# Kernel tuning notes

Measured on AMD Instinct MI355X. Metric: run time of the kernel, lower is better.

The kernel has to match this reference:

```python
import jax, jax.numpy as jnp
import numpy as np

HIDDEN = 128
SIGMA_A = 15.0
FACTOR_A = 180.0 / (SIGMA_A * np.pi)  # 180/(sigma_a*pi)


def _sinusoidal_embedding(indices, d_model):
    # torch: omegas = idx.view(-1,1,1)*div_term.view(1,-1,1); cat([sin,cos],dim=2)
    # -> interleaved [sin0, cos0, sin1, cos1, ...]
    div_term = jnp.exp(jnp.arange(0, d_model, 2, dtype=jnp.float32) * (-np.log(10000.0) / d_model))
    omegas = indices[..., None] * div_term  # (*, d/2)
    emb = jnp.stack([jnp.sin(omegas), jnp.cos(omegas)], axis=-1)  # (*, d/2, 2)
    return emb.reshape(*indices.shape, d_model)


def setup_inputs() -> dict:
    key = jax.random.key(0)
    k1, k2, k3 = jax.random.split(key, 3)
    B, N = 1, 1024
    points = jax.random.normal(k1, (B, N, 3), dtype=jnp.float32)
    normals = jax.random.normal(k2, (B, N, 3), dtype=jnp.float32)
    W = jax.random.normal(k3, (HIDDEN, HIDDEN), dtype=jnp.float32) / np.sqrt(HIDDEN)
    b = jnp.zeros((HIDDEN,), dtype=jnp.float32)
    return {"points": points, "normals": normals, "W": W, "b": b}


def reference(points, normals, W, b):
    # pairwise angle between normal_i (ref) and normal_j (anc), k=1 so mean over k is a no-op
    ref = normals[:, :, None, :]   # (B,N,1,3) -> n_i
    anc = normals[:, None, :, :]   # (B,1,N,3) -> n_j
    cross = jnp.cross(ref, anc)                    # (B,N,N,3)
    sin_v = jnp.linalg.norm(cross, axis=-1)        # (B,N,N)
    cos_v = jnp.sum(ref * anc, axis=-1)            # (B,N,N)
    angles = jnp.arctan2(sin_v, cos_v)
    a_indices = angles * FACTOR_A
    a_emb = _sinusoidal_embedding(a_indices, HIDDEN)  # (B,N,N,HIDDEN)
    a_emb = jax.lax.stop_gradient(a_emb)  # torch: no_grad + detach
    return a_emb @ W.T + b                # nn.Linear
```

## Files before the change

kernel.cpp:

```cpp
#include <hip/hip_runtime.h>
#include <math.h>


#define N_PTS 1024
#define HID   128
#define K_TAB 127
#define A_MAX 12.0f
#define T_OF_ANGLE 40.1070456591f
#define NEG_LOG1E4_OVER_128 (-0.0719557841f)

__global__ __launch_bounds__(128) void build_table(
        const float* __restrict__ W,
        const float* __restrict__ b,
        float* __restrict__ T) {
    __shared__ float ss[64], sc[64];
    const int t = blockIdx.x;
    const float a = (float)t * (A_MAX / (float)(K_TAB - 1));
    const int k = threadIdx.x;
    if (k < 64) {
        float omega = expf((float)(2 * k) * NEG_LOG1E4_OVER_128);
        ss[k] = sinf(a * omega);
        sc[k] = cosf(a * omega);
    }
    __syncthreads();
    float acc = b[k];
    const float* wrow = W + k * HID;
#pragma unroll 8
    for (int m = 0; m < 64; ++m) {
        acc += ss[m] * wrow[2 * m] + sc[m] * wrow[2 * m + 1];
    }
    T[t * HID + k] = acc;
}

__global__ __launch_bounds__(256) void fused_out(
        const float* __restrict__ normals,
        const float* __restrict__ T,
        float* __restrict__ out) {
    __shared__ float lt[K_TAB * HID];
    for (int idx = threadIdx.x; idx < (K_TAB * HID) / 4; idx += 256)
        ((float4*)lt)[idx] = ((const float4*)T)[idx];
    __syncthreads();

    const int lane = threadIdx.x & 63;
    const int half = lane >> 5;
    const int l32  = lane & 31;
    const int gwave = (blockIdx.x * 256 + threadIdx.x) >> 6;
    const int nwave = (gridDim.x * 256) >> 6;

    for (int base = gwave * 64; base < N_PTS * N_PTS; base += nwave * 64) {
        const int p = base + lane;
        const int i = p >> 10;
        const int j = p & 1023;
        float ax = normals[3 * i],  ay = normals[3 * i + 1], az = normals[3 * i + 2];
        float bx = normals[3 * j],  by = normals[3 * j + 1], bz = normals[3 * j + 2];
        float cx = ay * bz - az * by;
        float cy = az * bx - ax * bz;
        float cz = ax * by - ay * bx;
        float sv = sqrtf(cx * cx + cy * cy + cz * cz);
        float cv = ax * bx + ay * by + az * bz;
        float tval = atan2f(sv, cv) * T_OF_ANGLE;

        float* orow = out + (size_t)(base + half) * HID + l32 * 4;
#pragma unroll 4
        for (int k = 0; k < 32; ++k) {
            float t = __shfl(tval, 2 * k + half, 64);
            int idx = (int)t;
            idx = idx > K_TAB - 2 ? K_TAB - 2 : idx;
            float frac = t - (float)idx;
            const float4 v0 = *(const float4*)(lt + idx * HID + l32 * 4);
            const float4 v1 = *(const float4*)(lt + idx * HID + HID + l32 * 4);
            float4 r;
            r.x = fmaf(frac, v1.x - v0.x, v0.x);
            r.y = fmaf(frac, v1.y - v0.y, v0.y);
            r.z = fmaf(frac, v1.z - v0.z, v0.z);
            r.w = fmaf(frac, v1.w - v0.w, v0.w);
            *(float4*)orow = r;
            orow += 2 * HID;
        }
    }
}

extern "C" void kernel_launch(void* const* d_in, const int* in_sizes, int n_in,
                              void* d_out, int out_size, void* d_ws, size_t ws_size,
                              hipStream_t stream) {
    const float* normals = (const float*)d_in[1];
    const float* W       = (const float*)d_in[2];
    const float* b       = (const float*)d_in[3];
    float* out           = (float*)d_out;

    float* T = (float*)d_ws;

    build_table<<<K_TAB, 128, 0, stream>>>(W, b, T);
    fused_out<<<512, 256, 0, stream>>>(normals, T, out);
}
```

Baseline: 523.3 us.

## Store lookup table in fp16 LDS, interpolate with half2, restructure loop

Converts the shared-memory interpolation table to fp16, which halves LDS footprint and read bandwidth, and does the lerp with packed half2 FMA. The grid grows to 1024 blocks with a fixed 4-iteration outer loop, and launch bounds are set for higher occupancy. Per-point indices and fractions are now precomputed and broadcast with readlane instead of shuffles. This trades accuracy (fp16 table values and fractions) for lower LDS pressure and more blocks resident per CU, while the 4 MB-per-row fp32 output writes remain the main cost.

```diff
diff --git a/kernel.cpp b/kernel.cpp
--- a/kernel.cpp
+++ b/kernel.cpp
@@ -1,4 +1,5 @@
 #include <hip/hip_runtime.h>
+#include <hip/hip_fp16.h>
 #include <math.h>
 
 
@@ -8,6 +9,8 @@
 #define A_MAX 12.0f
 #define T_OF_ANGLE 40.1070456591f
 #define NEG_LOG1E4_OVER_128 (-0.0719557841f)
+#define GRID_B 1024
+#define OUTER  4
 
 __global__ __launch_bounds__(128) void build_table(
         const float* __restrict__ W,
@@ -32,49 +35,74 @@
     T[t * HID + k] = acc;
 }
 
-__global__ __launch_bounds__(256) void fused_out(
+__global__ __launch_bounds__(256, 4) void fused_out(
         const float* __restrict__ normals,
         const float* __restrict__ T,
         float* __restrict__ out) {
-    __shared__ float lt[K_TAB * HID];
-    for (int idx = threadIdx.x; idx < (K_TAB * HID) / 4; idx += 256)
-        ((float4*)lt)[idx] = ((const float4*)T)[idx];
+    __shared__ __half lt[K_TAB * HID];
+    for (int c = threadIdx.x; c < (K_TAB * HID) / 4; c += 256) {
+        float4 v = ((const float4*)T)[c];
+        ((__half2*)lt)[2 * c]     = __floats2half2_rn(v.x, v.y);
+        ((__half2*)lt)[2 * c + 1] = __floats2half2_rn(v.z, v.w);
+    }
     __syncthreads();
 
-    const int lane = threadIdx.x & 63;
-    const int half = lane >> 5;
-    const int l32  = lane & 31;
+    const int lane  = threadIdx.x & 63;
+    const int hsel  = lane >> 5;
+    const int l32   = lane & 31;
     const int gwave = (blockIdx.x * 256 + threadIdx.x) >> 6;
-    const int nwave = (gridDim.x * 256) >> 6;
+    const int STRIDE = GRID_B * 4 * 64;
 
-    for (int base = gwave * 64; base < N_PTS * N_PTS; base += nwave * 64) {
-        const int p = base + lane;
+    int rowb_[OUTER];
+    int frb_[OUTER];
+#pragma unroll
+    for (int o = 0; o < OUTER; ++o) {
+        const int p = gwave * 64 + o * STRIDE + lane;
         const int i = p >> 10;
         const int j = p & 1023;
-        float ax = normals[3 * i],  ay = normals[3 * i + 1], az = normals[3 * i + 2];
-        float bx = normals[3 * j],  by = normals[3 * j + 1], bz = normals[3 * j + 2];
+        float ax = normals[3 * i], ay = normals[3 * i + 1], az = normals[3 * i + 2];
+        float bx = normals[3 * j], by = normals[3 * j + 1], bz = normals[3 * j + 2];
         float cx = ay * bz - az * by;
         float cy = az * bx - ax * bz;
         float cz = ax * by - ay * bx;
         float sv = sqrtf(cx * cx + cy * cy + cz * cz);
         float cv = ax * bx + ay * by + az * bz;
-        float tval = atan2f(sv, cv) * T_OF_ANGLE;
+        float t  = atan2f(sv, cv) * T_OF_ANGLE;
+        int idx = (int)t;
+        idx = idx > K_TAB - 2 ? K_TAB - 2 : idx;
+        float frac = t - (float)idx;
+        rowb_[o] = idx * (HID * 2);
+        __half2 f2 = __float2half2_rn(frac);
+        frb_[o] = __builtin_bit_cast(int, f2);
+    }
 
-        float* orow = out + (size_t)(base + half) * HID + l32 * 4;
-#pragma unroll 4
+    const char* ltb = (const char*)lt;
+    const int laneoff = l32 * 8;
+#pragma unroll
+    for (int o = 0; o < OUTER; ++o) {
+        float* orow = out + (size_t)(gwave * 64 + o * STRIDE + hsel) * HID + l32 * 4;
+#pragma unroll
         for (int k = 0; k < 32; ++k) {
-            float t = __shfl(tval, 2 * k + half, 64);
-            int idx = (int)t;
-            idx = idx > K_TAB - 2 ? K_TAB - 2 : idx;
-            float frac = t - (float)idx;
-            const float4 v0 = *(const float4*)(lt + idx * HID + l32 * 4);
-            const float4 v1 = *(const float4*)(lt + idx * HID + HID + l32 * 4);
-            float4 r;
-            r.x = fmaf(frac, v1.x - v0.x, v0.x);
-            r.y = fmaf(frac, v1.y - v0.y, v0.y);
-            r.z = fmaf(frac, v1.z - v0.z, v0.z);
-            r.w = fmaf(frac, v1.w - v0.w, v0.w);
-            *(float4*)orow = r;
+            int rb0 = __builtin_amdgcn_readlane(rowb_[o], 2 * k);
+            int rb1 = __builtin_amdgcn_readlane(rowb_[o], 2 * k + 1);
+            int fb0 = __builtin_amdgcn_readlane(frb_[o], 2 * k);
+            int fb1 = __builtin_amdgcn_readlane(frb_[o], 2 * k + 1);
+            int rb = hsel ? rb1 : rb0;
+            int fb = hsel ? fb1 : fb0;
+            const char* pa = ltb + rb + laneoff;
+            uint2 ua = *(const uint2*)(pa);
+            uint2 ub = *(const uint2*)(pa + HID * 2);
+            __half2 a0 = __builtin_bit_cast(__half2, ua.x);
+            __half2 a1 = __builtin_bit_cast(__half2, ua.y);
+            __half2 b0 = __builtin_bit_cast(__half2, ub.x);
+            __half2 b1 = __builtin_bit_cast(__half2, ub.y);
+            __half2 fr2 = __builtin_bit_cast(__half2, fb);
+            __half2 r0 = __hfma2(fr2, __hsub2(b0, a0), a0);
+            __half2 r1 = __hfma2(fr2, __hsub2(b1, a1), a1);
+            float2 f0 = __half22float2(r0);
+            float2 f1 = __half22float2(r1);
+            float4 rv = make_float4(f0.x, f0.y, f1.x, f1.y);
+            *(float4*)orow = rv;
             orow += 2 * HID;
         }
     }
@@ -91,5 +119,5 @@
     float* T = (float*)d_ws;
 
     build_table<<<K_TAB, 128, 0, stream>>>(W, b, T);
-    fused_out<<<512, 256, 0, stream>>>(normals, T, out);
+    fused_out<<<GRID_B, 256, 0, stream>>>(normals, T, out);
 }
```

Measured after the change: 521.6 us. About the same (-0.3%).
